# Performance work log

Measured on AMD Instinct MI355X. Metric: run time of the kernel, lower is better.

Reference implementation:

```python
import jax, jax.numpy as jnp
import numpy as np

M1, M2, M3 = 12, 12, 8
WIDTH = 32


def _spectral_conv(v, wr, wi):
    # v: [B, C, X, Y, T]; wr/wi: [4, Ci, Co, M1, M2, M3]
    B, C, X, Y, T = v.shape
    vft = jnp.fft.rfftn(v, axes=(-3, -2, -1))  # [B,C,X,Y,T//2+1] complex
    w = wr.astype(jnp.complex64) + 1j * wi.astype(jnp.complex64)
    mul = lambda blk, ww: jnp.einsum('bixyz,ioxyz->boxyz', blk, ww)
    out = jnp.zeros((B, wr.shape[2], X, Y, T // 2 + 1), dtype=vft.dtype)
    out = out.at[:, :, :M1, :M2, :M3].set(mul(vft[:, :, :M1, :M2, :M3], w[0]))
    out = out.at[:, :, -M1:, :M2, :M3].set(mul(vft[:, :, -M1:, :M2, :M3], w[1]))
    out = out.at[:, :, :M1, -M2:, :M3].set(mul(vft[:, :, :M1, -M2:, :M3], w[2]))
    out = out.at[:, :, -M1:, -M2:, :M3].set(mul(vft[:, :, -M1:, -M2:, :M3], w[3]))
    return jnp.fft.irfftn(out, s=(X, Y, T), axes=(-3, -2, -1))


def _conv1x1(v, w, b):
    # v: [B,C,X,Y,T]; w: [Co,Ci]; b: [Co]
    return jnp.einsum('bixyz,oi->boxyz', v, w) + b[None, :, None, None, None]


def setup_inputs() -> dict:
    key = jax.random.key(0)
    ks = jax.random.split(key, 24)
    B, X, Y, T = 8, 64, 64, 40
    W = WIDTH
    scale = 1.0 / (W * W)
    d = {}
    d['h'] = jax.random.normal(ks[0], (B, X, Y, T, 2), dtype=jnp.float32)
    d['x'] = jax.random.normal(ks[1], (B, X, Y, T, 3), dtype=jnp.float32)
    d['fc0_w'] = jax.random.normal(ks[2], (5, W), dtype=jnp.float32) * 0.3
    d['fc0_b'] = jnp.zeros((W,), dtype=jnp.float32)
    for i, name in enumerate(['sc0', 'sc1', 'sc3']):
        d[name + '_wr'] = scale * jax.random.uniform(ks[3 + 2 * i], (4, W, W, M1, M2, M3), dtype=jnp.float32)
        d[name + '_wi'] = scale * jax.random.uniform(ks[4 + 2 * i], (4, W, W, M1, M2, M3), dtype=jnp.float32)
    for i, name in enumerate(['w0', 'w1', 'w3']):
        d[name + '_w'] = jax.random.normal(ks[9 + 2 * i], (W, W), dtype=jnp.float32) * (1.0 / np.sqrt(W))
        d[name + '_b'] = jnp.zeros((W,), dtype=jnp.float32)
    d['fc1_w'] = jax.random.normal(ks[15], (W, 64), dtype=jnp.float32) * (1.0 / np.sqrt(W))
    d['fc1_b'] = jnp.zeros((64,), dtype=jnp.float32)
    d['fc2_w'] = jax.random.normal(ks[16], (64, 2), dtype=jnp.float32) * 0.125
    d['fc2_b'] = jnp.zeros((2,), dtype=jnp.float32)
    return d


def reference(h, x, fc0_w, fc0_b, sc0_wr, sc0_wi, sc1_wr, sc1_wi, sc3_wr, sc3_wi,
              w0_w, w0_b, w1_w, w1_b, w3_w, w3_b, fc1_w, fc1_b, fc2_w, fc2_b):
    v = jnp.concatenate((h, x), axis=-1)                 # [B,X,Y,T,5]
    v = v @ fc0_w + fc0_b                                # lift to width
    v = jnp.transpose(v, (0, 4, 1, 2, 3))                # [B,W,X,Y,T]
    v = jax.nn.gelu(_spectral_conv(v, sc0_wr, sc0_wi) + _conv1x1(v, w0_w, w0_b), approximate=False)
    v = jax.nn.gelu(_spectral_conv(v, sc1_wr, sc1_wi) + _conv1x1(v, w1_w, w1_b), approximate=False)
    v = _spectral_conv(v, sc3_wr, sc3_wi) + _conv1x1(v, w3_w, w3_b)
    v = jnp.transpose(v, (0, 2, 3, 4, 1))                # [B,X,Y,T,W]
    v = jax.nn.gelu(v @ fc1_w + fc1_b, approximate=False)
    return v @ fc2_w + fc2_b                             # [B,X,Y,T,2]
```

## Files before the change

### kernel.cpp

```cpp
#include <hip/hip_runtime.h>
#include <math.h>

#define BATCH 8
#define WID   32
#define NX    64
#define NY    64
#define NT    40
#define M1C   12
#define KT    8
#define KXC   24
#define KYC   24
#define NXY   (NX*NY)
#define NXYT  (NXY*NT)
#define NP    (BATCH*NXYT)

#define TWO_PI 6.283185307179586f

static __device__ __forceinline__ float gelu_f(float v){
  return 0.5f*v*(1.0f + erff(v*0.7071067811865476f));
}

static __device__ __forceinline__ void barrier_lds(){
  asm volatile("s_waitcnt lgkmcnt(0)\n\ts_barrier" ::: "memory");
}


__global__ __launch_bounds__(256) void k_fc0(const float* __restrict__ h, const float* __restrict__ x,
                                             const float* __restrict__ w, const float* __restrict__ b,
                                             float* __restrict__ V){
  __shared__ float sw[160], sb[32];
  int tid=threadIdx.x;
  if(tid<160) sw[tid]=w[tid];
  if(tid<32)  sb[tid]=b[tid];
  __syncthreads();
  int pl = tid>>3, q = tid&7;
  int p = blockIdx.x*32 + pl;
  float i0=h[(size_t)p*2], i1=h[(size_t)p*2+1];
  float i2=x[(size_t)p*3], i3=x[(size_t)p*3+1], i4=x[(size_t)p*3+2];
  int c0=q*4;
  float4 o;
  float* po=(float*)&o;
  #pragma unroll
  for(int u=0;u<4;u++){
    int c=c0+u;
    po[u] = sb[c] + i0*sw[c] + i1*sw[32+c] + i2*sw[64+c] + i3*sw[96+c] + i4*sw[128+c];
  }
  ((float4*)V)[(size_t)p*8 + q] = o;
}

__global__ __launch_bounds__(512) void k_fwd_ty(const float* __restrict__ V, float2* __restrict__ F2){
  __shared__ __align__(16) unsigned char smem[55296];
  float2* twy   = (float2*)(smem+43008);
  float2* f2out = (float2*)smem;
  int tid = threadIdx.x;
  int h = tid >> 8, t8 = tid & 255;
  int b = blockIdx.x >> 6, x = blockIdx.x & 63;
  int c = t8 & 31, k = t8 >> 5;
  for(int i=tid;i<KYC*NY;i+=512){
    int ky=i>>6, y=i&63;
    int f = ky<M1C ? ky : ky+40;
    float ang = -TWO_PI*(float)((f*y)%NY)/(float)NY;
    twy[i] = make_float2(cosf(ang), sinf(ang));
  }
  float2 twr[20];
  #pragma unroll
  for(int t=0;t<20;t++){
    float ang = -TWO_PI*(float)((k*t)%NT)/(float)NT;
    twr[t] = make_float2(cosf(ang), sinf(ang));
  }
  float sgn = (k&1) ? -1.0f : 1.0f;
  int toff = (k&1)*20;
  float2 acc[KYC];
  #pragma unroll
  for(int q=0;q<KYC;q++) acc[q]=make_float2(0.f,0.f);
  const float4* src = (const float4*)(V + (size_t)(b*NX+x)*(NY*NT*WID));
  float* myb0 = (float*)(smem + h*21504);
  float* myb1 = myb0 + 2688;

  int s0 = t8;
  int c40 = s0&7, t0s = (s0>>3)%20, yl0 = s0/160;
  bool has1 = (t8 < 64);
  int s1 = t8 + 256;
  int c41 = s1&7, t1s = (s1>>3)%20, yl1 = s1/160;

  float4 pa0, pb0, pa1, pb1;
  pa0 = src[(2*h + yl0)*320 + t0s*8 + c40];
  pb0 = src[(2*h + yl0)*320 + t0s*8 + c40 + 160];
  if(has1){
    pa1 = src[(2*h + yl1)*320 + t1s*8 + c41];
    pb1 = src[(2*h + yl1)*320 + t1s*8 + c41 + 160];
  }
  {
    float* bse = myb0 + yl0*1344 + t0s;
    #pragma unroll
    for(int e=0;e<4;e++){
      float av=((float*)&pa0)[e], bv=((float*)&pb0)[e];
      bse[(4*c40+e)*42]      = av+bv;
      bse[(4*c40+e)*42 + 20] = av-bv;
    }
    if(has1){
      float* bs1 = myb0 + yl1*1344 + t1s;
      #pragma unroll
      for(int e=0;e<4;e++){
        float av=((float*)&pa1)[e], bv=((float*)&pb1)[e];
        bs1[(4*c41+e)*42]      = av+bv;
        bs1[(4*c41+e)*42 + 20] = av-bv;
      }
    }
  }
  pa0 = src[(2*(h+2) + yl0)*320 + t0s*8 + c40];
  pb0 = src[(2*(h+2) + yl0)*320 + t0s*8 + c40 + 160];
  if(has1){
    pa1 = src[(2*(h+2) + yl1)*320 + t1s*8 + c41];
    pb1 = src[(2*(h+2) + yl1)*320 + t1s*8 + c41 + 160];
  }
  __syncthreads();

  #pragma unroll 1
  for(int it=0; it<16; ++it){
    int g = 2*it + h;
    const float* vb = (it&1) ? myb1 : myb0;
    float*       vn = (it&1) ? myb0 : myb1;
    if(it+1<16){
      float* bse = vn + yl0*1344 + t0s;
      #pragma unroll
      for(int e=0;e<4;e++){
        float av=((float*)&pa0)[e], bv=((float*)&pb0)[e];
        bse[(4*c40+e)*42]      = av+bv;
        bse[(4*c40+e)*42 + 20] = av-bv;
      }
      if(has1){
        float* bs1 = vn + yl1*1344 + t1s;
        #pragma unroll
        for(int e=0;e<4;e++){
          float av=((float*)&pa1)[e], bv=((float*)&pb1)[e];
          bs1[(4*c41+e)*42]      = av+bv;
          bs1[(4*c41+e)*42 + 20] = av-bv;
        }
      }
      if(it+2<16){
        const float4* sg = src + (size_t)(2*(g+4))*320;
        pa0 = sg[yl0*320 + t0s*8 + c40];
        pb0 = sg[yl0*320 + t0s*8 + c40 + 160];
        if(has1){
          pa1 = sg[yl1*320 + t1s*8 + c41];
          pb1 = sg[yl1*320 + t1s*8 + c41 + 160];
        }
      }
    }
    {
      const float* vp0 = vb + c*42 + toff;
      const float* vp1 = vp0 + 1344;
      float sr0=0.f,si0=0.f,sr1=0.f,si1=0.f;
      #pragma unroll
      for(int i5=0; i5<5; i5++){
        float2 a0 = *(const float2*)(vp0 + i5*4);
        float2 b0 = *(const float2*)(vp0 + i5*4 + 2);
        float2 a1 = *(const float2*)(vp1 + i5*4);
        float2 b1 = *(const float2*)(vp1 + i5*4 + 2);
        float2 w0=twr[i5*4], w1=twr[i5*4+1], w2=twr[i5*4+2], w3=twr[i5*4+3];
        sr0 += a0.x*w0.x + a0.y*w1.x + b0.x*w2.x + b0.y*w3.x;
        si0 += a0.x*w0.y + a0.y*w1.y + b0.x*w2.y + b0.y*w3.y;
        sr1 += a1.x*w0.x + a1.y*w1.x + b1.x*w2.x + b1.y*w3.x;
        si1 += a1.x*w0.y + a1.y*w1.y + b1.x*w2.y + b1.y*w3.y;
      }
      int y = 2*g;
      #pragma unroll
      for(int q=0;q<KYC;q++){
        float4 wy = *(const float4*)&twy[q*NY + y];
        acc[q].x += sr0*wy.x - si0*wy.y + sr1*wy.z - si1*wy.w;
        acc[q].y += sr0*wy.y + si0*wy.x + sr1*wy.w + si1*wy.z;
      }
    }
    barrier_lds();
  }
  (void)sgn;
  if(h==0){
    #pragma unroll
    for(int q=0;q<KYC;q++) f2out[c*193 + q*8 + k] = acc[q];
  }
  __syncthreads();
  if(h==1){
    #pragma unroll
    for(int q=0;q<KYC;q++){
      float2 v = f2out[c*193 + q*8 + k];
      f2out[c*193 + q*8 + k] = make_float2(v.x+acc[q].x, v.y+acc[q].y);
    }
  }
  __syncthreads();
  for(int i=tid;i<WID*KYC*KT;i+=512){
    int cc=i/192, e=i-cc*192;
    F2[((size_t)(b*WID+cc)*NX + x)*(KYC*KT) + e] = f2out[cc*193 + e];
  }
}

__global__ __launch_bounds__(256) void k_fwd_x(const float2* __restrict__ F2, float2* __restrict__ F3){
  __shared__ float2 tile[NX*KT];
  __shared__ float2 twi[KXC*65];
  int tid=threadIdx.x;
  int bc = blockIdx.x / KYC;
  int ky = blockIdx.x - bc*KYC;
  for(int i=tid;i<NX*KT;i+=256){
    int xx=i/KT, kt=i-xx*KT;
    tile[i] = F2[((size_t)bc*NX + xx)*(KYC*KT) + ky*KT + kt];
  }
  for(int i=tid;i<KXC*NX;i+=256){
    int kx=i/NX, xx=i-kx*NX;
    int f = kx<M1C ? kx : kx+40;
    float ang = -TWO_PI*(float)((f*xx)%NX)/(float)NX;
    twi[kx*65+xx] = make_float2(cosf(ang), sinf(ang));
  }
  __syncthreads();
  for(int item=tid; item<KXC*KT; item+=256){
    int kx=item/KT, kt=item-kx*KT;
    float sr=0.f, si=0.f;
    #pragma unroll 8
    for(int xx=0;xx<NX;xx++){
      float2 a = tile[xx*KT+kt];
      float2 w = twi[kx*65+xx];
      sr += a.x*w.x - a.y*w.y;
      si += a.x*w.y + a.y*w.x;
    }
    F3[(size_t)bc*(KXC*KYC*KT) + kx*(KYC*KT) + ky*KT + kt] = make_float2(sr,si);
  }
}

__global__ __launch_bounds__(256) void k_mix(const float2* __restrict__ F3, const float* __restrict__ wr,
                                             const float* __restrict__ wi, float2* __restrict__ F4){
  __shared__ float2 f3s[BATCH*WID*KT];
  int tid = threadIdx.x;
  int kx = blockIdx.x / KYC, ky = blockIdx.x - kx*KYC;
  int mode0 = blockIdx.x * KT;
  int xp = (kx>=M1C), yp = (ky>=M1C);
  int m1 = kx - M1C*xp, m2 = ky - M1C*yp;
  int blk = xp + 2*yp;
  for(int i=tid;i<1024;i+=256){
    int row=i>>2, q=i&3;
    ((float4*)f3s)[row*4+q] = ((const float4*)(F3 + (size_t)row*4608 + mode0))[q];
  }
  int o = tid>>3, kt = tid&7;
  size_t wbase = (size_t)blk*1179648 + (size_t)o*1152 + m1*96 + m2*8 + kt;
  float wre[WID], wim[WID];
  #pragma unroll
  for(int i=0;i<WID;i++){
    wre[i] = wr[wbase + (size_t)i*36864];
    wim[i] = wi[wbase + (size_t)i*36864];
  }
  __syncthreads();
  #pragma unroll
  for(int b=0;b<BATCH;b++){
    float ar=0.f, ai=0.f;
    #pragma unroll
    for(int i=0;i<WID;i++){
      float2 a = f3s[(b*WID+i)*KT + kt];
      ar += a.x*wre[i] - a.y*wim[i];
      ai += a.x*wim[i] + a.y*wre[i];
    }
    F4[(size_t)(b*WID+o)*4608 + mode0 + kt] = make_float2(ar,ai);
  }
}

__global__ __launch_bounds__(256) void k_inv_x(const float2* __restrict__ F4, float2* __restrict__ F2){
  __shared__ float2 tile[KXC*KT];
  __shared__ float2 twi[NX*25];
  int tid=threadIdx.x;
  int bc = blockIdx.x / KYC, ky = blockIdx.x - (blockIdx.x/KYC)*KYC;
  for(int i=tid;i<KXC*KT;i+=256){
    int kx=i/KT, kt=i-kx*KT;
    tile[i] = F4[(size_t)bc*4608 + kx*(KYC*KT) + ky*KT + kt];
  }
  for(int i=tid;i<NX*KXC;i+=256){
    int xx=i/KXC, kx=i-xx*KXC;
    int f = kx<M1C ? kx : kx+40;
    float ang = TWO_PI*(float)((f*xx)%NX)/(float)NX;
    twi[xx*25+kx] = make_float2(cosf(ang)*(1.0f/64.0f), sinf(ang)*(1.0f/64.0f));
  }
  __syncthreads();
  for(int item=tid; item<NX*KT; item+=256){
    int xx=item/KT, kt=item-xx*KT;
    float sr=0.f, si=0.f;
    #pragma unroll 8
    for(int kx=0;kx<KXC;kx++){
      float2 a = tile[kx*KT+kt];
      float2 w = twi[xx*25+kx];
      sr += a.x*w.x - a.y*w.y;
      si += a.x*w.y + a.y*w.x;
    }
    F2[((size_t)bc*NX + xx)*(KYC*KT) + ky*KT + kt] = make_float2(sr,si);
  }
}

template<bool GELU>
__global__ __launch_bounds__(256) void k_conv(const float2* __restrict__ F2, const float* __restrict__ wcv,
                                              const float* __restrict__ bcv, float* __restrict__ V){
  __shared__ __align__(16) unsigned char smem[34816];
  float*  vtA  = (float*)smem;
  float*  vtB  = (float*)(smem+10240);
  float2* ftc0 = (float2*)(smem+20480);
  float2* ftc1 = (float2*)(smem+24576);
  float2* twy  = (float2*)(smem+28672);
  float2* f2h  = (float2*)smem;

  int tid=threadIdx.x;
  int b  = blockIdx.x >> 7;
  int x  = (blockIdx.x >> 1) & 63;
  int y0 = (blockIdx.x & 1) * 32;
  int cid = tid & 31, ktid = tid >> 5;
  int oid = tid & 31, tg  = tid >> 5;

  float2 fr[KYC];
  #pragma unroll
  for(int half=0; half<2; half++){
    for(int i=tid;i<1536;i+=256){
      int cc=i/96, q=i-cc*96;
      ((float4*)f2h)[i] = *((const float4*)(F2 + ((size_t)(b*WID + half*16 + cc)*NX + x)*(KYC*KT)) + q);
    }
    __syncthreads();
    if((cid>>4) == half){
      const float2* fp = f2h + (cid&15)*192 + ktid;
      #pragma unroll
      for(int ky=0;ky<KYC;ky++) fr[ky] = fp[ky*8];
    }
    __syncthreads();
  }
  {
    float ts = (ktid==0 ? 1.0f : 2.0f) * (1.0f/(float)NT);
    #pragma unroll
    for(int ky=0;ky<KYC;ky++){ fr[ky].x *= ts; fr[ky].y *= ts; }
  }
  float wreg[WID];
  #pragma unroll
  for(int cc=0;cc<WID;cc++) wreg[cc] = wcv[oid*WID + cc];
  float breg = bcv[oid];
  float2 twtg[KT];
  #pragma unroll
  for(int k=0;k<KT;k++){
    float ang = 0.78539816339744831f*(float)((k*tg)&7);
    twtg[k] = make_float2(cosf(ang), sinf(ang));
  }
  for(int i=tid;i<32*KYC;i+=256){
    int yy=i/KYC, ky=i-yy*KYC;
    int f = ky<M1C ? ky : ky+40;
    float ang = TWO_PI*(float)((f*(y0+yy))%NY)/(float)NY;
    twy[i] = make_float2(cosf(ang)*(1.0f/64.0f), sinf(ang)*(1.0f/64.0f));
  }
  float* plane = V + (size_t)((b*NX+x)*NY + y0)*(NT*WID);
  const float4* gp = (const float4*)plane;
  bool has3 = tid < 128;
  {
    float4 p0 = gp[tid], p1 = gp[256+tid];
    float4 p2 = has3 ? gp[512+tid] : make_float4(0,0,0,0);
    ((float4*)vtA)[tid] = p0;
    ((float4*)vtA)[256+tid] = p1;
    if(has3) ((float4*)vtA)[512+tid] = p2;
  }
  float4 rA = gp[640+tid], rB = gp[640+256+tid];
  float4 rC = has3 ? gp[640+512+tid] : make_float4(0,0,0,0);
  __syncthreads();

  constexpr float CJ[KT][5] = {
    {1.f, 1.f,          1.f,          1.f,          1.f         },
    {1.f, 0.98768834f,  0.95105652f,  0.89100652f,  0.80901699f },
    {1.f, 0.95105652f,  0.80901699f,  0.58778525f,  0.30901699f },
    {1.f, 0.89100652f,  0.58778525f,  0.15643447f, -0.30901699f },
    {1.f, 0.80901699f,  0.30901699f, -0.30901699f, -0.80901699f },
    {1.f, 0.70710678f,  0.f,         -0.70710678f, -1.f         },
    {1.f, 0.58778525f, -0.30901699f, -0.95105652f, -0.80901699f },
    {1.f, 0.45399050f, -0.58778525f, -0.98768834f, -0.30901699f },
  };
  constexpr float SJ[KT][5] = {
    {0.f, 0.f,          0.f,          0.f,          0.f         },
    {0.f, 0.15643447f,  0.30901699f,  0.45399050f,  0.58778525f },
    {0.f, 0.30901699f,  0.58778525f,  0.80901699f,  0.95105652f },
    {0.f, 0.45399050f,  0.80901699f,  0.98768834f,  0.95105652f },
    {0.f, 0.58778525f,  0.95105652f,  0.95105652f,  0.58778525f },
    {0.f, 0.70710678f,  1.f,          0.70710678f,  0.f         },
    {0.f, 0.80901699f,  0.95105652f,  0.30901699f, -0.58778525f },
    {0.f, 0.89100652f,  0.80901699f, -0.15643447f, -0.95105652f },
  };

  #pragma unroll 1
  for(int it=0; it<16; ++it){
    float*  vcur = (it&1) ? vtB  : vtA;
    float*  vnxt = (it&1) ? vtA  : vtB;
    float2* fcur = (it&1) ? ftc1 : ftc0;
    int yl = it*2;
    {
      const float2* tw0 = twy + (size_t)yl*KYC;
      const float2* tw1 = tw0 + KYC;
      float sr0=0.f, si0=0.f, sr1=0.f, si1=0.f;
      #pragma unroll
      for(int ky=0;ky<KYC;ky+=2){
        float2 a  = fr[ky];
        float2 b2 = fr[ky+1];
        float4 w0 = *(const float4*)&tw0[ky];
        float4 w1 = *(const float4*)&tw1[ky];
        sr0 += a.x*w0.x - a.y*w0.y + b2.x*w0.z - b2.y*w0.w;
        si0 += a.x*w0.y + a.y*w0.x + b2.x*w0.w + b2.y*w0.z;
        sr1 += a.x*w1.x - a.y*w1.y + b2.x*w1.z - b2.y*w1.w;
        si1 += a.x*w1.y + a.y*w1.x + b2.x*w1.w + b2.y*w1.z;
      }
      fcur[      ktid*32 + cid] = make_float2(sr0,si0);
      fcur[256 + ktid*32 + cid] = make_float2(sr1,si1);
    }
    barrier_lds();
    if(it+1 < 16){
      ((float4*)vnxt)[tid] = rA;
      ((float4*)vnxt)[256+tid] = rB;
      if(has3) ((float4*)vnxt)[512+tid] = rC;
    }
    if(it+2 < 16){
      const float4* q = gp + (size_t)(it+2)*640;
      rA = q[tid]; rB = q[256+tid];
      if(has3) rC = q[512+tid];
    }
    #pragma unroll
    for(int yy=0; yy<2; yy++){
      const float2* fsrc = fcur + yy*256;
      const float*  vb   = vcur + yy*1280;
      float* outp = plane + (size_t)(yl+yy)*(NT*WID);
      float acc[5];
      #pragma unroll
      for(int j=0;j<5;j++) acc[j] = breg;
      #pragma unroll
      for(int k=0;k<KT;k++){
        float2 f = fsrc[k*32 + oid];
        float gx = f.x*twtg[k].x - f.y*twtg[k].y;
        float gy = f.x*twtg[k].y + f.y*twtg[k].x;
        #pragma unroll
        for(int j=0;j<5;j++) acc[j] += gx*CJ[k][j] - gy*SJ[k][j];
      }
      #pragma unroll
      for(int j=0;j<5;j++){
        int t = tg*5 + j;
        float a = acc[j];
        const float* vrow = vb + t*32;
        #pragma unroll
        for(int c4=0;c4<WID;c4+=4){
          float4 vv = *(const float4*)(vrow + c4);
          a += vv.x*wreg[c4] + vv.y*wreg[c4+1] + vv.z*wreg[c4+2] + vv.w*wreg[c4+3];
        }
        outp[t*32 + oid] = GELU ? gelu_f(a) : a;
      }
    }
  }
}

__global__ __launch_bounds__(256) void k_mlp(const float* __restrict__ V, const float* __restrict__ w1,
                                             const float* __restrict__ b1, const float* __restrict__ w2,
                                             const float* __restrict__ b2, float* __restrict__ out){
  __shared__ float sw1t[64*WID];
  __shared__ float sb1[64], sw2[128], sb2[2];
  int tid=threadIdx.x;
  for(int i=tid;i<64*WID;i+=256){ int j=i>>5, c=i&31; sw1t[i]=w1[c*64+j]; }
  if(tid<64) sb1[tid]=b1[tid];
  if(tid<128) sw2[tid]=w2[tid];
  if(tid<2) sb2[tid]=b2[tid];
  __syncthreads();
  size_t p0 = (size_t)blockIdx.x*1024 + (size_t)tid*4;
  float vv[128];
  const float4* vp = (const float4*)(V + p0*WID);
  #pragma unroll
  for(int q=0;q<32;q++) *((float4*)(vv+4*q)) = vp[q];
  float oa[8];
  #pragma unroll
  for(int pt=0;pt<4;pt++){ oa[2*pt]=sb2[0]; oa[2*pt+1]=sb2[1]; }
  #pragma unroll 4
  for(int j=0;j<64;j++){
    float a0=sb1[j], a1=a0, a2=a0, a3=a0;
    const float* wrow = sw1t + j*WID;
    #pragma unroll
    for(int c4=0;c4<WID;c4+=4){
      float4 w = *(const float4*)(wrow + c4);
      a0 += vv[     c4]*w.x + vv[     c4+1]*w.y + vv[     c4+2]*w.z + vv[     c4+3]*w.w;
      a1 += vv[32 + c4]*w.x + vv[32 + c4+1]*w.y + vv[32 + c4+2]*w.z + vv[32 + c4+3]*w.w;
      a2 += vv[64 + c4]*w.x + vv[64 + c4+1]*w.y + vv[64 + c4+2]*w.z + vv[64 + c4+3]*w.w;
      a3 += vv[96 + c4]*w.x + vv[96 + c4+1]*w.y + vv[96 + c4+2]*w.z + vv[96 + c4+3]*w.w;
    }
    a0=gelu_f(a0); a1=gelu_f(a1); a2=gelu_f(a2); a3=gelu_f(a3);
    float u0=sw2[2*j], u1=sw2[2*j+1];
    oa[0]+=a0*u0; oa[1]+=a0*u1; oa[2]+=a1*u0; oa[3]+=a1*u1;
    oa[4]+=a2*u0; oa[5]+=a2*u1; oa[6]+=a3*u0; oa[7]+=a3*u1;
  }
  float4* op = (float4*)(out + p0*2);
  op[0]=make_float4(oa[0],oa[1],oa[2],oa[3]);
  op[1]=make_float4(oa[4],oa[5],oa[6],oa[7]);
}

extern "C" void kernel_launch(void* const* d_in, const int* in_sizes, int n_in,
                              void* d_out, int out_size, void* d_ws, size_t ws_size,
                              hipStream_t stream){
  const float* h     = (const float*)d_in[0];
  const float* x     = (const float*)d_in[1];
  const float* fc0_w = (const float*)d_in[2];
  const float* fc0_b = (const float*)d_in[3];
  const float* scwr[3] = {(const float*)d_in[4], (const float*)d_in[6], (const float*)d_in[8]};
  const float* scwi[3] = {(const float*)d_in[5], (const float*)d_in[7], (const float*)d_in[9]};
  const float* cw[3]   = {(const float*)d_in[10], (const float*)d_in[12], (const float*)d_in[14]};
  const float* cb[3]   = {(const float*)d_in[11], (const float*)d_in[13], (const float*)d_in[15]};
  const float* fc1_w = (const float*)d_in[16];
  const float* fc1_b = (const float*)d_in[17];
  const float* fc2_w = (const float*)d_in[18];
  const float* fc2_b = (const float*)d_in[19];

  const size_t VSZ = (size_t)BATCH*WID*NXYT;
  float*  V  = (float*)d_ws;
  float2* F2 = (float2*)(V + VSZ);
  float2* F4 = F2 + (size_t)BATCH*WID*NX*KYC*KT;
  float2* F3 = (float2*)d_out;

  k_fc0<<<NP/32, 256, 0, stream>>>(h, x, fc0_w, fc0_b, V);
  for(int L=0; L<3; L++){
    k_fwd_ty<<<BATCH*NX, 512, 0, stream>>>(V, F2);
    k_fwd_x<<<(BATCH*WID)*KYC, 256, 0, stream>>>(F2, F3);
    k_mix<<<KXC*KYC, 256, 0, stream>>>(F3, scwr[L], scwi[L], F4);
    k_inv_x<<<(BATCH*WID)*KYC, 256, 0, stream>>>(F4, F2);
    if(L<2) k_conv<true ><<<BATCH*NX*2, 256, 0, stream>>>(F2, cw[L], cb[L], V);
    else    k_conv<false><<<BATCH*NX*2, 256, 0, stream>>>(F2, cw[L], cb[L], V);
  }
  k_mlp<<<NP/1024, 256, 0, stream>>>(V, fc1_w, fc1_b, fc2_w, fc2_b, (float*)d_out);
}
```

Before: 1.393 ms.

## Fuse fc0 lift into first-layer forward FFT and conv kernels

Removes the standalone fc0 lift kernel. The first layer's forward t/y DFT kernel and its 1x1 conv kernel now read the raw h and x inputs and compute the 5-to-32 lift on the fly from weights held in shared memory. This avoids writing and then twice re-reading the 32-channel lifted tensor for layer 0, at the cost of recomputing the lift in two kernels plus extra ALU work and strided scalar loads of x.

```diff
diff --git a/kernel.cpp b/kernel.cpp
--- a/kernel.cpp
+++ b/kernel.cpp
@@ -25,37 +25,22 @@
 }
 
 
-__global__ __launch_bounds__(256) void k_fc0(const float* __restrict__ h, const float* __restrict__ x,
-                                             const float* __restrict__ w, const float* __restrict__ b,
-                                             float* __restrict__ V){
-  __shared__ float sw[160], sb[32];
-  int tid=threadIdx.x;
-  if(tid<160) sw[tid]=w[tid];
-  if(tid<32)  sb[tid]=b[tid];
-  __syncthreads();
-  int pl = tid>>3, q = tid&7;
-  int p = blockIdx.x*32 + pl;
-  float i0=h[(size_t)p*2], i1=h[(size_t)p*2+1];
-  float i2=x[(size_t)p*3], i3=x[(size_t)p*3+1], i4=x[(size_t)p*3+2];
-  int c0=q*4;
-  float4 o;
-  float* po=(float*)&o;
-  #pragma unroll
-  for(int u=0;u<4;u++){
-    int c=c0+u;
-    po[u] = sb[c] + i0*sw[c] + i1*sw[32+c] + i2*sw[64+c] + i3*sw[96+c] + i4*sw[128+c];
-  }
-  ((float4*)V)[(size_t)p*8 + q] = o;
-}
-
-__global__ __launch_bounds__(512) void k_fwd_ty(const float* __restrict__ V, float2* __restrict__ F2){
-  __shared__ __align__(16) unsigned char smem[55296];
+template<bool LIFT>
+__global__ __launch_bounds__(512) void k_fwd_ty(const float* __restrict__ V, float2* __restrict__ F2,
+                                                const float* __restrict__ hin, const float* __restrict__ xin,
+                                                const float* __restrict__ lw, const float* __restrict__ lb){
+  __shared__ __align__(16) unsigned char smem[56320];
   float2* twy   = (float2*)(smem+43008);
   float2* f2out = (float2*)smem;
+  float*  wTl   = (float*)(smem+55296);
   int tid = threadIdx.x;
   int h = tid >> 8, t8 = tid & 255;
   int b = blockIdx.x >> 6, x = blockIdx.x & 63;
   int c = t8 & 31, k = t8 >> 5;
+  if constexpr(LIFT){
+    if(tid<192){ int cc=tid/6, i=tid-6*cc; wTl[cc*8+i] = (i<5)? lw[i*32+cc] : lb[cc]; }
+    __syncthreads();
+  }
   for(int i=tid;i<KYC*NY;i+=512){
     int ky=i>>6, y=i&63;
     int f = ky<M1C ? ky : ky+40;
@@ -68,12 +53,13 @@
     float ang = -TWO_PI*(float)((k*t)%NT)/(float)NT;
     twr[t] = make_float2(cosf(ang), sinf(ang));
   }
-  float sgn = (k&1) ? -1.0f : 1.0f;
   int toff = (k&1)*20;
   float2 acc[KYC];
   #pragma unroll
   for(int q=0;q<KYC;q++) acc[q]=make_float2(0.f,0.f);
   const float4* src = (const float4*)(V + (size_t)(b*NX+x)*(NY*NT*WID));
+  const float* hb = hin + (size_t)(b*NX+x)*(NY*NT)*2;
+  const float* xb = xin + (size_t)(b*NX+x)*(NY*NT)*3;
   float* myb0 = (float*)(smem + h*21504);
   float* myb1 = myb0 + 2688;
 
@@ -84,36 +70,79 @@
   int c41 = s1&7, t1s = (s1>>3)%20, yl1 = s1/160;
 
   float4 pa0, pb0, pa1, pb1;
-  pa0 = src[(2*h + yl0)*320 + t0s*8 + c40];
-  pb0 = src[(2*h + yl0)*320 + t0s*8 + c40 + 160];
-  if(has1){
-    pa1 = src[(2*h + yl1)*320 + t1s*8 + c41];
-    pb1 = src[(2*h + yl1)*320 + t1s*8 + c41 + 160];
-  }
-  {
-    float* bse = myb0 + yl0*1344 + t0s;
-    #pragma unroll
-    for(int e=0;e<4;e++){
-      float av=((float*)&pa0)[e], bv=((float*)&pb0)[e];
-      bse[(4*c40+e)*42]      = av+bv;
-      bse[(4*c40+e)*42 + 20] = av-bv;
-    }
-    if(has1){
-      float* bs1 = myb0 + yl1*1344 + t1s;
-      #pragma unroll
-      for(int e=0;e<4;e++){
-        float av=((float*)&pa1)[e], bv=((float*)&pb1)[e];
-        bs1[(4*c41+e)*42]      = av+bv;
-        bs1[(4*c41+e)*42 + 20] = av-bv;
-      }
-    }
-  }
-  pa0 = src[(2*(h+2) + yl0)*320 + t0s*8 + c40];
-  pb0 = src[(2*(h+2) + yl0)*320 + t0s*8 + c40 + 160];
-  if(has1){
-    pa1 = src[(2*(h+2) + yl1)*320 + t1s*8 + c41];
-    pb1 = src[(2*(h+2) + yl1)*320 + t1s*8 + c41 + 160];
-  }
+  float2 hA0,hB0,hA1,hB1;
+  float xA00,xA01,xA02,xB00,xB01,xB02;
+  float xA10,xA11,xA12,xB10,xB11,xB12;
+
+#define TY_LOAD(G) do{ \
+    if constexpr(LIFT){ \
+      { size_t pt = (size_t)((2*(G)+yl0)*40 + t0s); \
+        hA0 = *(const float2*)(hb + pt*2); \
+        hB0 = *(const float2*)(hb + (pt+20)*2); \
+        xA00 = xb[pt*3]; xA01 = xb[pt*3+1]; xA02 = xb[pt*3+2]; \
+        xB00 = xb[(pt+20)*3]; xB01 = xb[(pt+20)*3+1]; xB02 = xb[(pt+20)*3+2]; } \
+      if(has1){ size_t pt = (size_t)((2*(G)+yl1)*40 + t1s); \
+        hA1 = *(const float2*)(hb + pt*2); \
+        hB1 = *(const float2*)(hb + (pt+20)*2); \
+        xA10 = xb[pt*3]; xA11 = xb[pt*3+1]; xA12 = xb[pt*3+2]; \
+        xB10 = xb[(pt+20)*3]; xB11 = xb[(pt+20)*3+1]; xB12 = xb[(pt+20)*3+2]; } \
+    } else { \
+      pa0 = src[(2*(G) + yl0)*320 + t0s*8 + c40]; \
+      pb0 = src[(2*(G) + yl0)*320 + t0s*8 + c40 + 160]; \
+      if(has1){ \
+        pa1 = src[(2*(G) + yl1)*320 + t1s*8 + c41]; \
+        pb1 = src[(2*(G) + yl1)*320 + t1s*8 + c41 + 160]; \
+      } \
+    } \
+  }while(0)
+
+#define TY_STAGE(BUF) do{ \
+    if constexpr(LIFT){ \
+      float su0=hA0.x+hB0.x, su1=hA0.y+hB0.y, su2=xA00+xB00, su3=xA01+xB01, su4=xA02+xB02; \
+      float sd0=hA0.x-hB0.x, sd1=hA0.y-hB0.y, sd2=xA00-xB00, sd3=xA01-xB01, sd4=xA02-xB02; \
+      float* bse = (BUF) + yl0*1344 + t0s; \
+      _Pragma("unroll") \
+      for(int e=0;e<4;e++){ \
+        const float* wr = wTl + (4*c40+e)*8; \
+        float4 w03 = *(const float4*)wr; float2 w45 = *(const float2*)(wr+4); \
+        bse[(4*c40+e)*42]      = 2.f*w45.y + su0*w03.x + su1*w03.y + su2*w03.z + su3*w03.w + su4*w45.x; \
+        bse[(4*c40+e)*42 + 20] = sd0*w03.x + sd1*w03.y + sd2*w03.z + sd3*w03.w + sd4*w45.x; \
+      } \
+      if(has1){ \
+        float tu0=hA1.x+hB1.x, tu1=hA1.y+hB1.y, tu2=xA10+xB10, tu3=xA11+xB11, tu4=xA12+xB12; \
+        float td0=hA1.x-hB1.x, td1=hA1.y-hB1.y, td2=xA10-xB10, td3=xA11-xB11, td4=xA12-xB12; \
+        float* bs1 = (BUF) + yl1*1344 + t1s; \
+        _Pragma("unroll") \
+        for(int e=0;e<4;e++){ \
+          const float* wr = wTl + (4*c41+e)*8; \
+          float4 w03 = *(const float4*)wr; float2 w45 = *(const float2*)(wr+4); \
+          bs1[(4*c41+e)*42]      = 2.f*w45.y + tu0*w03.x + tu1*w03.y + tu2*w03.z + tu3*w03.w + tu4*w45.x; \
+          bs1[(4*c41+e)*42 + 20] = td0*w03.x + td1*w03.y + td2*w03.z + td3*w03.w + td4*w45.x; \
+        } \
+      } \
+    } else { \
+      float* bse = (BUF) + yl0*1344 + t0s; \
+      _Pragma("unroll") \
+      for(int e=0;e<4;e++){ \
+        float av=((float*)&pa0)[e], bv=((float*)&pb0)[e]; \
+        bse[(4*c40+e)*42]      = av+bv; \
+        bse[(4*c40+e)*42 + 20] = av-bv; \
+      } \
+      if(has1){ \
+        float* bs1 = (BUF) + yl1*1344 + t1s; \
+        _Pragma("unroll") \
+        for(int e=0;e<4;e++){ \
+          float av=((float*)&pa1)[e], bv=((float*)&pb1)[e]; \
+          bs1[(4*c41+e)*42]      = av+bv; \
+          bs1[(4*c41+e)*42 + 20] = av-bv; \
+        } \
+      } \
+    } \
+  }while(0)
+
+  TY_LOAD(h);
+  TY_STAGE(myb0);
+  TY_LOAD(h+2);
   __syncthreads();
 
   #pragma unroll 1
@@ -122,30 +151,9 @@
     const float* vb = (it&1) ? myb1 : myb0;
     float*       vn = (it&1) ? myb0 : myb1;
     if(it+1<16){
-      float* bse = vn + yl0*1344 + t0s;
-      #pragma unroll
-      for(int e=0;e<4;e++){
-        float av=((float*)&pa0)[e], bv=((float*)&pb0)[e];
-        bse[(4*c40+e)*42]      = av+bv;
-        bse[(4*c40+e)*42 + 20] = av-bv;
-      }
-      if(has1){
-        float* bs1 = vn + yl1*1344 + t1s;
-        #pragma unroll
-        for(int e=0;e<4;e++){
-          float av=((float*)&pa1)[e], bv=((float*)&pb1)[e];
-          bs1[(4*c41+e)*42]      = av+bv;
-          bs1[(4*c41+e)*42 + 20] = av-bv;
-        }
-      }
+      TY_STAGE(vn);
       if(it+2<16){
-        const float4* sg = src + (size_t)(2*(g+4))*320;
-        pa0 = sg[yl0*320 + t0s*8 + c40];
-        pb0 = sg[yl0*320 + t0s*8 + c40 + 160];
-        if(has1){
-          pa1 = sg[yl1*320 + t1s*8 + c41];
-          pb1 = sg[yl1*320 + t1s*8 + c41 + 160];
-        }
+        TY_LOAD(g+4);
       }
     }
     {
@@ -174,7 +182,6 @@
     }
     barrier_lds();
   }
-  (void)sgn;
   if(h==0){
     #pragma unroll
     for(int q=0;q<KYC;q++) f2out[c*193 + q*8 + k] = acc[q];
@@ -192,6 +199,8 @@
     int cc=i/192, e=i-cc*192;
     F2[((size_t)(b*WID+cc)*NX + x)*(KYC*KT) + e] = f2out[cc*193 + e];
   }
+#undef TY_LOAD
+#undef TY_STAGE
 }
 
 __global__ __launch_bounds__(256) void k_fwd_x(const float2* __restrict__ F2, float2* __restrict__ F3){
@@ -290,15 +299,18 @@
   }
 }
 
-template<bool GELU>
+template<bool GELU, bool LIFT>
 __global__ __launch_bounds__(256) void k_conv(const float2* __restrict__ F2, const float* __restrict__ wcv,
-                                              const float* __restrict__ bcv, float* __restrict__ V){
-  __shared__ __align__(16) unsigned char smem[34816];
+                                              const float* __restrict__ bcv, float* __restrict__ V,
+                                              const float* __restrict__ hin, const float* __restrict__ xin,
+                                              const float* __restrict__ lw, const float* __restrict__ lb){
+  __shared__ __align__(16) unsigned char smem[35840];
   float*  vtA  = (float*)smem;
   float*  vtB  = (float*)(smem+10240);
   float2* ftc0 = (float2*)(smem+20480);
   float2* ftc1 = (float2*)(smem+24576);
   float2* twy  = (float2*)(smem+28672);
+  float*  wTl  = (float*)(smem+34816);
   float2* f2h  = (float2*)smem;
 
   int tid=threadIdx.x;
@@ -308,6 +320,10 @@
   int cid = tid & 31, ktid = tid >> 5;
   int oid = tid & 31, tg  = tid >> 5;
 
+  if constexpr(LIFT){
+    if(tid<192){ int cc=tid/6, i=tid-6*cc; wTl[cc*8+i] = (i<5)? lw[i*32+cc] : lb[cc]; }
+  }
+
   float2 fr[KYC];
   #pragma unroll
   for(int half=0; half<2; half++){
@@ -346,16 +362,61 @@
   }
   float* plane = V + (size_t)((b*NX+x)*NY + y0)*(NT*WID);
   const float4* gp = (const float4*)plane;
+  const float* hbc = hin + (size_t)((b*NX+x)*NY + y0)*NT*2;
+  const float* xbc = xin + (size_t)((b*NX+x)*NY + y0)*NT*3;
   bool has3 = tid < 128;
-  {
-    float4 p0 = gp[tid], p1 = gp[256+tid];
-    float4 p2 = has3 ? gp[512+tid] : make_float4(0,0,0,0);
-    ((float4*)vtA)[tid] = p0;
-    ((float4*)vtA)[256+tid] = p1;
-    if(has3) ((float4*)vtA)[512+tid] = p2;
-  }
-  float4 rA = gp[640+tid], rB = gp[640+256+tid];
-  float4 rC = has3 ? gp[640+512+tid] : make_float4(0,0,0,0);
+  int t0c = tid>>3;
+  int yy1c = (tid>=64);
+  int t1c = yy1c ? ((tid-64)>>3) : ((tid+256)>>3);
+  int t2c = (tid+192)>>3;
+  int c4c = tid&7;
+
+  float4 rA, rB, rC;
+  float2 hC0, hC1, hC2;
+  float xC00,xC01,xC02,xC10,xC11,xC12,xC20,xC21,xC22;
+
+#define CV_LOAD(P) do{ \
+    if constexpr(LIFT){ \
+      { size_t pt = (size_t)((2*(P))*40 + t0c); \
+        hC0 = *(const float2*)(hbc + pt*2); \
+        xC00 = xbc[pt*3]; xC01 = xbc[pt*3+1]; xC02 = xbc[pt*3+2]; } \
+      { size_t pt = (size_t)((2*(P)+yy1c)*40 + t1c); \
+        hC1 = *(const float2*)(hbc + pt*2); \
+        xC10 = xbc[pt*3]; xC11 = xbc[pt*3+1]; xC12 = xbc[pt*3+2]; } \
+      if(has3){ size_t pt = (size_t)((2*(P)+1)*40 + t2c); \
+        hC2 = *(const float2*)(hbc + pt*2); \
+        xC20 = xbc[pt*3]; xC21 = xbc[pt*3+1]; xC22 = xbc[pt*3+2]; } \
+    } else { \
+      const float4* q = gp + (size_t)(P)*640; \
+      rA = q[tid]; rB = q[256+tid]; \
+      if(has3) rC = q[512+tid]; \
+    } \
+  }while(0)
+
+#define CV_STAGE(BUF) do{ \
+    if constexpr(LIFT){ \
+      float4 v0, v1, v2; \
+      _Pragma("unroll") \
+      for(int e=0;e<4;e++){ \
+        const float* wr = wTl + (4*c4c+e)*8; \
+        float4 w03 = *(const float4*)wr; float2 w45 = *(const float2*)(wr+4); \
+        ((float*)&v0)[e] = w45.y + hC0.x*w03.x + hC0.y*w03.y + xC00*w03.z + xC01*w03.w + xC02*w45.x; \
+        ((float*)&v1)[e] = w45.y + hC1.x*w03.x + hC1.y*w03.y + xC10*w03.z + xC11*w03.w + xC12*w45.x; \
+        if(has3) ((float*)&v2)[e] = w45.y + hC2.x*w03.x + hC2.y*w03.y + xC20*w03.z + xC21*w03.w + xC22*w45.x; \
+      } \
+      ((float4*)(BUF))[tid] = v0; \
+      ((float4*)(BUF))[256+tid] = v1; \
+      if(has3) ((float4*)(BUF))[512+tid] = v2; \
+    } else { \
+      ((float4*)(BUF))[tid] = rA; \
+      ((float4*)(BUF))[256+tid] = rB; \
+      if(has3) ((float4*)(BUF))[512+tid] = rC; \
+    } \
+  }while(0)
+
+  CV_LOAD(0);
+  CV_STAGE(vtA);
+  CV_LOAD(1);
   __syncthreads();
 
   constexpr float CJ[KT][5] = {
@@ -405,14 +466,10 @@
     }
     barrier_lds();
     if(it+1 < 16){
-      ((float4*)vnxt)[tid] = rA;
-      ((float4*)vnxt)[256+tid] = rB;
-      if(has3) ((float4*)vnxt)[512+tid] = rC;
+      CV_STAGE(vnxt);
     }
     if(it+2 < 16){
-      const float4* q = gp + (size_t)(it+2)*640;
-      rA = q[tid]; rB = q[256+tid];
-      if(has3) rC = q[512+tid];
+      CV_LOAD(it+2);
     }
     #pragma unroll
     for(int yy=0; yy<2; yy++){
@@ -444,6 +501,8 @@
       }
     }
   }
+#undef CV_LOAD
+#undef CV_STAGE
 }
 
 __global__ __launch_bounds__(256) void k_mlp(const float* __restrict__ V, const float* __restrict__ w1,
@@ -509,14 +568,15 @@
   float2* F4 = F2 + (size_t)BATCH*WID*NX*KYC*KT;
   float2* F3 = (float2*)d_out;
 
-  k_fc0<<<NP/32, 256, 0, stream>>>(h, x, fc0_w, fc0_b, V);
   for(int L=0; L<3; L++){
-    k_fwd_ty<<<BATCH*NX, 512, 0, stream>>>(V, F2);
+    if(L==0) k_fwd_ty<true ><<<BATCH*NX, 512, 0, stream>>>(V, F2, h, x, fc0_w, fc0_b);
+    else     k_fwd_ty<false><<<BATCH*NX, 512, 0, stream>>>(V, F2, h, x, fc0_w, fc0_b);
     k_fwd_x<<<(BATCH*WID)*KYC, 256, 0, stream>>>(F2, F3);
     k_mix<<<KXC*KYC, 256, 0, stream>>>(F3, scwr[L], scwi[L], F4);
     k_inv_x<<<(BATCH*WID)*KYC, 256, 0, stream>>>(F4, F2);
-    if(L<2) k_conv<true ><<<BATCH*NX*2, 256, 0, stream>>>(F2, cw[L], cb[L], V);
-    else    k_conv<false><<<BATCH*NX*2, 256, 0, stream>>>(F2, cw[L], cb[L], V);
+    if(L==0)      k_conv<true ,true ><<<BATCH*NX*2, 256, 0, stream>>>(F2, cw[0], cb[0], V, h, x, fc0_w, fc0_b);
+    else if(L==1) k_conv<true ,false><<<BATCH*NX*2, 256, 0, stream>>>(F2, cw[1], cb[1], V, h, x, fc0_w, fc0_b);
+    else          k_conv<false,false><<<BATCH*NX*2, 256, 0, stream>>>(F2, cw[2], cb[2], V, h, x, fc0_w, fc0_b);
   }
   k_mlp<<<NP/1024, 256, 0, stream>>>(V, fc1_w, fc1_b, fc2_w, fc2_b, (float*)d_out);
 }
```

New measurement: 1.425 ms. 2.3% more time.
